# Kernel optimization log

Hardware: AMD Instinct MI355X
Metric: run time of the kernel (lower is better)

## Reference

```python
import jax, jax.numpy as jnp
import numpy as np
import math

N, S, T, D = 4, 2048, 2048, 1024

def setup_inputs() -> dict:
    key = jax.random.key(0)
    ks = jax.random.split(key, 6)
    scale = 1.0 / math.sqrt(D)
    return {
        "query": jax.random.normal(ks[0], (N, S, D), dtype=jnp.float32),
        "key": jax.random.normal(ks[1], (N, T, D), dtype=jnp.float32),
        "value": jax.random.normal(ks[2], (N, T, D), dtype=jnp.float32),
        # causal mask: 1 = attend, 0 = masked out (masked_fill where mask == 0)
        "attn_mask": jnp.tril(jnp.ones((S, T), dtype=jnp.int32)),
        "Wq": jax.random.normal(ks[3], (D, D), dtype=jnp.float32) * scale,
        "Wk": jax.random.normal(ks[4], (D, D), dtype=jnp.float32) * scale,
        "Wv": jax.random.normal(ks[5], (D, D), dtype=jnp.float32) * scale,
    }

def reference(query, key, value, attn_mask, Wq, Wk, Wv):
    # nn.Linear(bias=False): y = x @ W.T
    q = jnp.einsum('nsd,ed->nse', query, Wq)
    k = jnp.einsum('ntd,ed->nte', key, Wk)
    v = jnp.einsum('ntd,ed->nte', value, Wv)
    # scaled dot-product scores [N, S, T]
    dot = jnp.einsum('nse,nte->nst', q, k) / jnp.sqrt(jnp.asarray(D, q.dtype))
    dot = jnp.where(attn_mask == 0, -jnp.inf, dot)
    scores = jax.nn.softmax(dot, axis=-1)
    # dropout is identity in eval mode
    y = jnp.einsum('nst,nte->nse', scores, v)
    return y
```

## Files before the change

### kernel.cpp

```cpp
#include <hip/hip_runtime.h>
#include <math.h>

using u16 = unsigned short;
typedef __attribute__((ext_vector_type(8))) __bf16 bf16x8;
typedef __attribute__((ext_vector_type(4))) float f32x4;
typedef __attribute__((ext_vector_type(4))) float f4v;
typedef __attribute__((ext_vector_type(8))) u16 u16x8;

__device__ __forceinline__ u16 f2bf(float f) {
  unsigned u = __float_as_uint(f);
  u += 0x7fffu + ((u >> 16) & 1u);
  return (u16)(u >> 16);
}

__device__ __forceinline__ void gload16(const void* g, void* l) {
  __builtin_amdgcn_global_load_lds(
      (const __attribute__((address_space(1))) unsigned int*)g,
      (__attribute__((address_space(3))) unsigned int*)l, 16, 0, 0);
}

__device__ __forceinline__ f32x4 MF(bf16x8 a, bf16x8 b, f32x4 c) {
  return __builtin_amdgcn_mfma_f32_16x16x32_bf16(a, b, c, 0, 0, 0);
}

#define BARX() __builtin_amdgcn_s_barrier()
#define LGKM0() asm volatile("s_waitcnt lgkmcnt(0)" ::: "memory")
#define VMW4() asm volatile("s_waitcnt vmcnt(4)" ::: "memory")
#define VMW0() asm volatile("s_waitcnt vmcnt(0)" ::: "memory")

__global__ __launch_bounds__(256) void prep(
    const float* __restrict__ q, const float* __restrict__ v,
    const float* __restrict__ k, const float* __restrict__ Wk,
    const float* __restrict__ Wq, const float* __restrict__ Wv,
    u16* __restrict__ qb, u16* __restrict__ wkT, u16* __restrict__ wqT,
    u16* __restrict__ wv_bf, float* __restrict__ lbuf) {
  __shared__ float t[64][65];
  int b = blockIdx.x;
  if (b < 6144) {
    int z = b >> 11;
    int bb = b & 2047;
    const float* in = (z == 0) ? q : (z == 1) ? v : k;
    size_t i = ((size_t)bb * 256 + threadIdx.x) * 16;
    f4v a0 = *reinterpret_cast<const f4v*>(in + i);
    f4v a1 = *reinterpret_cast<const f4v*>(in + i + 4);
    f4v a2 = *reinterpret_cast<const f4v*>(in + i + 8);
    f4v a3 = *reinterpret_cast<const f4v*>(in + i + 12);
    u16x8 r0, r1;
    r0[0] = f2bf(a0[0]); r0[1] = f2bf(a0[1]); r0[2] = f2bf(a0[2]); r0[3] = f2bf(a0[3]);
    r0[4] = f2bf(a1[0]); r0[5] = f2bf(a1[1]); r0[6] = f2bf(a1[2]); r0[7] = f2bf(a1[3]);
    r1[0] = f2bf(a2[0]); r1[1] = f2bf(a2[1]); r1[2] = f2bf(a2[2]); r1[3] = f2bf(a2[3]);
    r1[4] = f2bf(a3[0]); r1[5] = f2bf(a3[1]); r1[6] = f2bf(a3[2]); r1[7] = f2bf(a3[3]);
    u16* o = qb + (size_t)z * 8388608 + i;
    *reinterpret_cast<u16x8*>(o) = r0;
    *reinterpret_cast<u16x8*>(o + 8) = r1;
  } else if (b < 6656) {
    int c = b - 6144;
    int z = c >> 8, idx = c & 255;
    const float* I = z ? Wq : Wk;
    u16* O = z ? wqT : wkT;
    int c0 = (idx & 15) * 64, r0 = (idx >> 4) * 64;
    int tx = threadIdx.x & 63, ty = threadIdx.x >> 6;
    #pragma unroll
    for (int i = 0; i < 64; i += 4)
      t[ty + i][tx] = I[(size_t)(r0 + ty + i) * 1024 + c0 + tx];
    __syncthreads();
    #pragma unroll
    for (int i = 0; i < 64; i += 4)
      O[(size_t)(c0 + ty + i) * 1024 + r0 + tx] = f2bf(t[tx][ty + i]);
  } else if (b < 6912) {
    int bb = b - 6656;
    size_t i = (size_t)bb * 4096 + threadIdx.x * 16;
    #pragma unroll
    for (int h = 0; h < 2; ++h) {
      f4v a = *reinterpret_cast<const f4v*>(Wv + i + h * 8);
      f4v c = *reinterpret_cast<const f4v*>(Wv + i + h * 8 + 4);
      u16x8 r;
      r[0] = f2bf(a[0]); r[1] = f2bf(a[1]); r[2] = f2bf(a[2]); r[3] = f2bf(a[3]);
      r[4] = f2bf(c[0]); r[5] = f2bf(c[1]); r[6] = f2bf(c[2]); r[7] = f2bf(c[3]);
      *reinterpret_cast<u16x8*>(wv_bf + i + h * 8) = r;
    }
  } else {
    f4v z4 = {0.f, 0.f, 0.f, 0.f};
    #pragma unroll
    for (int j = 0; j < 8; ++j)
      *reinterpret_cast<f4v*>(&lbuf[threadIdx.x * 32 + j * 4]) = z4;
  }
}

__global__ __launch_bounds__(512, 1) void proj256(
    const u16* __restrict__ Xq, const u16* __restrict__ Xv,
    const u16* __restrict__ Mt, const u16* __restrict__ Wv,
    u16* __restrict__ Yq, u16* __restrict__ Vt) {
  int h = blockIdx.x;
  int l = (h & 7) * 32 + (h >> 3);
  const bool wV = l >= 128;
  int li = l & 127;
  int bm, bn;
  const u16 *Ag, *Bg;
  if (!wV) {
    bm = li >> 2; bn = li & 3;
    Ag = Xq + (size_t)bm * 256 * 1024;
    Bg = Mt + (size_t)bn * 256 * 1024;
  } else {
    bm = li & 3; bn = li >> 2;
    Ag = Wv + (size_t)bm * 256 * 1024;
    Bg = Xv + (size_t)bn * 256 * 1024;
  }

  __shared__ __align__(16) char sm[131072];

  const int tid = threadIdx.x;
  const int lane = tid & 63, wv = tid >> 6;
  const int wr = wv >> 2, wc = wv & 3;
  const int fr = lane & 15, hi = lane >> 4, fr7 = lane & 7;
  const int l3 = lane >> 3;
  const int colsw = ((lane & 7) ^ l3) * 8;
  const int lnx16 = lane * 16;

  const u16 *pA[2][2], *pB[2][2];
  int ldsA[2][2], ldsB[2][2];
  #pragma unroll
  for (int hh = 0; hh < 2; ++hh)
    #pragma unroll
    for (int j = 0; j < 2; ++j) {
      int row = hh * 128 + wv * 8 + j * 64 + l3;
      pA[hh][j] = Ag + (size_t)row * 1024 + colsw;
      pB[hh][j] = Bg + (size_t)row * 1024 + colsw;
      ldsA[hh][j] = hh * 16384 + (wv + j * 8) * 1024 + lnx16;
      ldsB[hh][j] = 32768 + ldsA[hh][j];
    }

  const int aBase = wr * 16384 + fr * 128;
  const int bBase = 32768 + (wc >> 1) * 16384 + ((wc & 1) * 64 + fr) * 128;
  const int sl0 = (hi ^ fr7) << 4;
  const int sl1 = ((4 + hi) ^ fr7) << 4;

#define RDA(buf, m, kk) (*(const bf16x8*)((buf) + aBase + (m) * 2048 + ((kk) ? sl1 : sl0)))
#define RDB(buf, n, kk) (*(const bf16x8*)((buf) + bBase + (n) * 2048 + ((kk) ? sl1 : sl0)))

  f32x4 acc[8][4] = {};
  const int nt = 16;

  {
    char* b0 = sm;
    gload16(pA[0][0], b0 + ldsA[0][0]); gload16(pA[0][1], b0 + ldsA[0][1]);
    gload16(pA[1][0], b0 + ldsA[1][0]); gload16(pA[1][1], b0 + ldsA[1][1]);
    gload16(pB[0][0], b0 + ldsB[0][0]); gload16(pB[0][1], b0 + ldsB[0][1]);
    gload16(pB[1][0], b0 + ldsB[1][0]); gload16(pB[1][1], b0 + ldsB[1][1]);
    char* b1 = sm + 65536;
    gload16(pB[0][0] + 64, b1 + ldsB[0][0]); gload16(pB[0][1] + 64, b1 + ldsB[0][1]);
    gload16(pB[1][0] + 64, b1 + ldsB[1][0]); gload16(pB[1][1] + 64, b1 + ldsB[1][1]);
  }
  VMW4();
  BARX();

  for (int t = 0; t < nt; ++t) {
    const int cur = t & 1;
    const char* buf = sm + cur * 65536;
    char* nbuf = sm + (cur ^ 1) * 65536;
    char* cbuf = sm + cur * 65536;
    const bool st1 = (t + 1 < nt), st2 = (t + 2 < nt);
    bf16x8 bf0[4], bf1[4];
    bf16x8 a00, a01, a10, a11;

    a00 = RDA(buf, 0, 0); a01 = RDA(buf, 0, 1);
    a10 = RDA(buf, 1, 0); a11 = RDA(buf, 1, 1);
    #pragma unroll
    for (int n = 0; n < 4; ++n) { bf0[n] = RDB(buf, n, 0); bf1[n] = RDB(buf, n, 1); }
    if (st1) {
      gload16(pA[0][0] + (t + 1) * 64, nbuf + ldsA[0][0]);
      gload16(pA[0][1] + (t + 1) * 64, nbuf + ldsA[0][1]);
    }
    BARX(); LGKM0();
    __builtin_amdgcn_s_setprio(1);
    #pragma unroll
    for (int n = 0; n < 4; ++n) {
      acc[0][n] = MF(a00, bf0[n], acc[0][n]);
      acc[0][n] = MF(a01, bf1[n], acc[0][n]);
      acc[1][n] = MF(a10, bf0[n], acc[1][n]);
      acc[1][n] = MF(a11, bf1[n], acc[1][n]);
    }
    __builtin_amdgcn_s_setprio(0);
    BARX();

    a00 = RDA(buf, 2, 0); a01 = RDA(buf, 2, 1);
    a10 = RDA(buf, 3, 0); a11 = RDA(buf, 3, 1);
    if (st1) {
      gload16(pA[1][0] + (t + 1) * 64, nbuf + ldsA[1][0]);
      gload16(pA[1][1] + (t + 1) * 64, nbuf + ldsA[1][1]);
    }
    if (st2) {
      gload16(pB[0][0] + (t + 2) * 64, cbuf + ldsB[0][0]);
      gload16(pB[0][1] + (t + 2) * 64, cbuf + ldsB[0][1]);
    }
    BARX(); LGKM0();
    __builtin_amdgcn_s_setprio(1);
    #pragma unroll
    for (int n = 0; n < 4; ++n) {
      acc[2][n] = MF(a00, bf0[n], acc[2][n]);
      acc[2][n] = MF(a01, bf1[n], acc[2][n]);
      acc[3][n] = MF(a10, bf0[n], acc[3][n]);
      acc[3][n] = MF(a11, bf1[n], acc[3][n]);
    }
    __builtin_amdgcn_s_setprio(0);
    BARX();

    a00 = RDA(buf, 4, 0); a01 = RDA(buf, 4, 1);
    a10 = RDA(buf, 5, 0); a11 = RDA(buf, 5, 1);
    if (st2) {
      gload16(pB[1][0] + (t + 2) * 64, cbuf + ldsB[1][0]);
      gload16(pB[1][1] + (t + 2) * 64, cbuf + ldsB[1][1]);
    }
    BARX(); LGKM0();
    __builtin_amdgcn_s_setprio(1);
    #pragma unroll
    for (int n = 0; n < 4; ++n) {
      acc[4][n] = MF(a00, bf0[n], acc[4][n]);
      acc[4][n] = MF(a01, bf1[n], acc[4][n]);
      acc[5][n] = MF(a10, bf0[n], acc[5][n]);
      acc[5][n] = MF(a11, bf1[n], acc[5][n]);
    }
    __builtin_amdgcn_s_setprio(0);
    BARX();

    a00 = RDA(buf, 6, 0); a01 = RDA(buf, 6, 1);
    a10 = RDA(buf, 7, 0); a11 = RDA(buf, 7, 1);
    if (st2) { VMW4(); } else if (st1) { VMW0(); }
    BARX(); LGKM0();
    __builtin_amdgcn_s_setprio(1);
    #pragma unroll
    for (int n = 0; n < 4; ++n) {
      acc[6][n] = MF(a00, bf0[n], acc[6][n]);
      acc[6][n] = MF(a01, bf1[n], acc[6][n]);
      acc[7][n] = MF(a10, bf0[n], acc[7][n]);
      acc[7][n] = MF(a11, bf1[n], acc[7][n]);
    }
    __builtin_amdgcn_s_setprio(0);
    BARX();
  }

  if (!wV) {
    const int row0 = bm * 256 + wr * 128 + hi * 4;
    const int col0 = bn * 256 + wc * 64 + fr;
    #pragma unroll
    for (int m = 0; m < 8; ++m)
      #pragma unroll
      for (int n = 0; n < 4; ++n)
        #pragma unroll
        for (int j = 0; j < 4; ++j)
          Yq[(size_t)(row0 + m * 16 + j) * 1024 + (col0 + n * 16)] =
              f2bf(acc[m][n][j]);
  } else {
    const int e0 = bm * 256 + wr * 128 + hi * 4;
    const int t0 = (bn & 7) * 256 + wc * 64 + fr;
    const size_t zoff = (size_t)(bn >> 3) * (1024 * 2048);
    #pragma unroll
    for (int m = 0; m < 8; ++m)
      #pragma unroll
      for (int n = 0; n < 4; ++n)
        #pragma unroll
        for (int j = 0; j < 4; ++j)
          Vt[zoff + (size_t)(e0 + m * 16 + j) * 2048 + (t0 + n * 16)] =
              f2bf(acc[m][n][j]);
  }
#undef RDA
#undef RDB
}

template<typename OutT, int MODE>
__global__ __launch_bounds__(512) void gemm_bt8(
    const u16* __restrict__ A, const u16* __restrict__ B, OutT* __restrict__ C,
    int K, int lda, int ldb, int ldc,
    size_t sA, size_t sB, size_t sC, float alpha, float* __restrict__ lbuf) {
  int bn, bm, bz = 0;
  int kEnd = K;
  if (MODE == 0) {
    bm = blockIdx.x >> 3;
    bn = blockIdx.x & 7;
  } else if (MODE == 1) {
    int h = blockIdx.x;
    int l = (h & 7) * 68 + (h >> 3);
    bz = l / 136;
    int t = l % 136;
    bm = (int)((sqrtf(8.f * (float)t + 1.f) - 1.f) * 0.5f);
    while ((bm + 1) * (bm + 2) / 2 <= t) ++bm;
    while (bm * (bm + 1) / 2 > t) --bm;
    bn = t - bm * (bm + 1) / 2;
  } else {
    int l = blockIdx.x;
    bm = 15 - (l >> 5);
    int rest = l & 31;
    bz = rest >> 3;
    bn = rest & 7;
    kEnd = (K < (bm + 1) * 128) ? K : (bm + 1) * 128;
  }
  const u16* Ag = A + sA * bz + (size_t)bm * 128 * lda;
  const u16* Bg = B + sB * bz + (size_t)bn * 128 * ldb;
  OutT* Cg = C + sC * bz;

  __shared__ __align__(16) u16 As[2][128 * 32];
  __shared__ __align__(16) u16 Bs[2][128 * 32];

  const int tid = threadIdx.x;
  const int lane = tid & 63, wv = tid >> 6;
  const int wr = wv >> 2, wc = wv & 3;
  const int fr = lane & 15, kq = (lane >> 4) * 8;
  const int g4 = (lane >> 4) * 4;

  const int e0 = wv * 512 + lane * 8;
  const int r0 = e0 >> 5, c0 = e0 & 31;
  const u16* a0 = Ag + (size_t)r0 * lda + c0;
  const u16* b0 = Bg + (size_t)r0 * ldb + c0;

  f32x4 acc[4][2] = {};
  const int nt = kEnd / 32;

  gload16(a0, &As[0][wv * 512]);
  gload16(b0, &Bs[0][wv * 512]);
  __syncthreads();

  for (int t = 0; t < nt; ++t) {
    const int cur = t & 1;
    if (t + 1 < nt) {
      const int k0 = (t + 1) * 32;
      gload16(a0 + k0, &As[cur ^ 1][wv * 512]);
      gload16(b0 + k0, &Bs[cur ^ 1][wv * 512]);
    }
    bf16x8 af[4], bfv[2];
    #pragma unroll
    for (int m = 0; m < 4; ++m)
      af[m] = *reinterpret_cast<const bf16x8*>(&As[cur][(wr * 64 + m * 16 + fr) * 32 + kq]);
    #pragma unroll
    for (int n = 0; n < 2; ++n)
      bfv[n] = *reinterpret_cast<const bf16x8*>(&Bs[cur][(wc * 32 + n * 16 + fr) * 32 + kq]);
    #pragma unroll
    for (int m = 0; m < 4; ++m)
      #pragma unroll
      for (int n = 0; n < 2; ++n)
        acc[m][n] = MF(af[m], bfv[n], acc[m][n]);
    __syncthreads();
  }

  if constexpr (MODE == 1) {
    float psum[4][4];
    #pragma unroll
    for (int m = 0; m < 4; ++m)
      #pragma unroll
      for (int j = 0; j < 4; ++j) {
        int tr = wr * 64 + g4 + m * 16 + j;
        float rs = 0.f;
        #pragma unroll
        for (int n = 0; n < 2; ++n) {
          int tc = wc * 32 + fr + n * 16;
          float p = 0.f;
          if (!(bm == bn && tc > tr)) p = __expf(acc[m][n][j] * alpha);
          Cg[(size_t)(bm * 128 + tr) * ldc + (bn * 128 + tc)] = f2bf(p);
          rs += p;
        }
        psum[m][j] = rs;
      }
    #pragma unroll
    for (int o = 1; o < 16; o <<= 1)
      #pragma unroll
      for (int m = 0; m < 4; ++m)
        #pragma unroll
        for (int j = 0; j < 4; ++j)
          psum[m][j] += __shfl_xor(psum[m][j], o, 64);
    float* lsum = (float*)As;
    if (fr == 0)
      #pragma unroll
      for (int m = 0; m < 4; ++m)
        #pragma unroll
        for (int j = 0; j < 4; ++j)
          lsum[wc * 128 + wr * 64 + g4 + m * 16 + j] = psum[m][j];
    __syncthreads();
    if (tid < 128) {
      float s = lsum[tid] + lsum[128 + tid] + lsum[256 + tid] + lsum[384 + tid];
      atomicAdd(&lbuf[(size_t)bz * 2048 + bm * 128 + tid], s);
    }
    return;
  }

  float il[4][4];
  if constexpr (MODE == 2) {
    #pragma unroll
    for (int m = 0; m < 4; ++m)
      #pragma unroll
      for (int j = 0; j < 4; ++j)
        il[m][j] = 1.0f / lbuf[(size_t)bz * 2048 + bm * 128 + wr * 64 + g4 + m * 16 + j];
  }

  const int row0 = bm * 128 + wr * 64 + g4;
  const int col0 = bn * 128 + wc * 32 + fr;
  #pragma unroll
  for (int m = 0; m < 4; ++m)
    #pragma unroll
    for (int n = 0; n < 2; ++n) {
      #pragma unroll
      for (int j = 0; j < 4; ++j) {
        float val;
        if constexpr (MODE == 2) val = acc[m][n][j] * il[m][j];
        else val = acc[m][n][j] * alpha;
        size_t idx = (size_t)(row0 + m * 16 + j) * ldc + (col0 + n * 16);
        if constexpr (sizeof(OutT) == 2) Cg[idx] = f2bf(val);
        else Cg[idx] = val;
      }
    }
}

extern "C" void kernel_launch(void* const* d_in, const int* in_sizes, int n_in,
                              void* d_out, int out_size, void* d_ws, size_t ws_size,
                              hipStream_t stream) {
  const float* q  = (const float*)d_in[0];
  const float* k  = (const float*)d_in[1];
  const float* v  = (const float*)d_in[2];
  const float* Wq = (const float*)d_in[4];
  const float* Wk = (const float*)d_in[5];
  const float* Wv = (const float*)d_in[6];
  float* out = (float*)d_out;
  char* ws = (char*)d_ws;

  const size_t MB = 1024ull * 1024ull;
  u16* sc   = (u16*)ws;
  u16* qb   = (u16*)ws;
  u16* xk   = (u16*)(ws + 32 * MB);
  u16* wsl  = (u16*)(ws + 48 * MB);
  u16* wkT  = (u16*)(ws + 52 * MB);
  u16* wqT  = (u16*)(ws + 54 * MB);
  u16* Vt   = (u16*)(ws + 56 * MB);
  u16* Yq   = (u16*)(ws + 72 * MB);
  float* lb = (float*)(ws + 88 * MB);
  (void)in_sizes; (void)n_in; (void)out_size; (void)ws_size;

  prep<<<6913, 256, 0, stream>>>(q, v, k, Wk, Wq, Wv, qb, wkT, wqT,
                                 wsl + 1048576, lb);

  gemm_bt8<u16, 0><<<64, 512, 0, stream>>>(
      wkT, wqT, wsl, 1024, 1024, 1024, 1024, 0, 0, 0, 1.0f, nullptr);

  proj256<<<256, 512, 0, stream>>>(qb, qb + 8388608, wsl, wsl + 1048576,
                                   Yq, Vt);

  gemm_bt8<u16, 1><<<544, 512, 0, stream>>>(
      Yq, xk, sc, 1024, 1024, 1024, 2048,
      (size_t)2048 * 1024, (size_t)2048 * 1024, (size_t)2048 * 2048, 0.03125f,
      lb);

  gemm_bt8<float, 2><<<512, 512, 0, stream>>>(
      sc, Vt, out, 2048, 2048, 2048, 1024,
      (size_t)2048 * 2048, (size_t)1024 * 2048, (size_t)2048 * 1024, 1.0f,
      lb);
}
```

Baseline: 156.6 us.

## Use 256x256 tiled GEMMs for scores and PV with split-K atomics

```diff
diff --git a/kernel.cpp b/kernel.cpp
--- a/kernel.cpp
+++ b/kernel.cpp
@@ -33,7 +33,7 @@
     const float* __restrict__ k, const float* __restrict__ Wk,
     const float* __restrict__ Wq, const float* __restrict__ Wv,
     u16* __restrict__ qb, u16* __restrict__ wkT, u16* __restrict__ wqT,
-    u16* __restrict__ wv_bf, float* __restrict__ lbuf) {
+    u16* __restrict__ wv_bf, float* __restrict__ lbuf, float* __restrict__ O) {
   __shared__ float t[64][65];
   int b = blockIdx.x;
   if (b < 6144) {
@@ -57,7 +57,7 @@
     int c = b - 6144;
     int z = c >> 8, idx = c & 255;
     const float* I = z ? Wq : Wk;
-    u16* O = z ? wqT : wkT;
+    u16* O2 = z ? wqT : wkT;
     int c0 = (idx & 15) * 64, r0 = (idx >> 4) * 64;
     int tx = threadIdx.x & 63, ty = threadIdx.x >> 6;
     #pragma unroll
@@ -66,7 +66,7 @@
     __syncthreads();
     #pragma unroll
     for (int i = 0; i < 64; i += 4)
-      O[(size_t)(c0 + ty + i) * 1024 + r0 + tx] = f2bf(t[tx][ty + i]);
+      O2[(size_t)(c0 + ty + i) * 1024 + r0 + tx] = f2bf(t[tx][ty + i]);
   } else if (b < 6912) {
     int bb = b - 6656;
     size_t i = (size_t)bb * 4096 + threadIdx.x * 16;
@@ -79,11 +79,20 @@
       r[4] = f2bf(c[0]); r[5] = f2bf(c[1]); r[6] = f2bf(c[2]); r[7] = f2bf(c[3]);
       *reinterpret_cast<u16x8*>(wv_bf + i + h * 8) = r;
     }
-  } else {
+  } else if (b == 6912) {
     f4v z4 = {0.f, 0.f, 0.f, 0.f};
     #pragma unroll
     for (int j = 0; j < 8; ++j)
       *reinterpret_cast<f4v*>(&lbuf[threadIdx.x * 32 + j * 4]) = z4;
+  } else {
+    int c = b - 6913;
+    int bz = c >> 8, bb = c & 255;
+    float* p = O + (size_t)bz * 2097152 + 1048576 +
+               (size_t)bb * 4096 + threadIdx.x * 16;
+    f4v z4 = {0.f, 0.f, 0.f, 0.f};
+    #pragma unroll
+    for (int j = 0; j < 4; ++j)
+      *reinterpret_cast<f4v*>(p + j * 4) = z4;
   }
 }
 
@@ -267,36 +276,244 @@
 #undef RDB
 }
 
-template<typename OutT, int MODE>
-__global__ __launch_bounds__(512) void gemm_bt8(
-    const u16* __restrict__ A, const u16* __restrict__ B, OutT* __restrict__ C,
-    int K, int lda, int ldb, int ldc,
-    size_t sA, size_t sB, size_t sC, float alpha, float* __restrict__ lbuf) {
-  int bn, bm, bz = 0;
-  int kEnd = K;
-  if (MODE == 0) {
-    bm = blockIdx.x >> 3;
-    bn = blockIdx.x & 7;
-  } else if (MODE == 1) {
-    int h = blockIdx.x;
-    int l = (h & 7) * 68 + (h >> 3);
-    bz = l / 136;
-    int t = l % 136;
-    bm = (int)((sqrtf(8.f * (float)t + 1.f) - 1.f) * 0.5f);
-    while ((bm + 1) * (bm + 2) / 2 <= t) ++bm;
-    while (bm * (bm + 1) / 2 > t) --bm;
-    bn = t - bm * (bm + 1) / 2;
+template<int MODE>
+__global__ __launch_bounds__(512, 1) void g256(
+    const u16* __restrict__ A, const u16* __restrict__ B,
+    u16* __restrict__ P, float* __restrict__ O, float* __restrict__ lbuf) {
+  int h = blockIdx.x;
+  int bm, bn, bz, nt, lda, ldb;
+  bool split = false;
+  const u16 *Ag, *Bg;
+  if (MODE == 1) {
+    int l = (h & 7) * 18 + (h >> 3);
+    bz = l / 36;
+    int tt = l % 36;
+    bm = (int)((sqrtf(8.f * tt + 1.f) - 1.f) * 0.5f);
+    while ((bm + 1) * (bm + 2) / 2 <= tt) ++bm;
+    while (bm * (bm + 1) / 2 > tt) --bm;
+    bn = tt - bm * (bm + 1) / 2;
+    lda = 1024; ldb = 1024; nt = 16;
+    Ag = A + (size_t)bz * 2097152 + (size_t)bm * 256 * 1024;
+    Bg = B + (size_t)bz * 2097152 + (size_t)bn * 256 * 1024;
   } else {
-    int l = blockIdx.x;
-    bm = 15 - (l >> 5);
-    int rest = l & 31;
-    bz = rest >> 3;
-    bn = rest & 7;
-    kEnd = (K < (bm + 1) * 128) ? K : (bm + 1) * 128;
-  }
-  const u16* Ag = A + sA * bz + (size_t)bm * 128 * lda;
-  const u16* Bg = B + sB * bz + (size_t)bn * 128 * ldb;
-  OutT* Cg = C + sC * bz;
+    int l = (h & 7) * 24 + (h >> 3);
+    bz = l / 48;
+    int r = l % 48;
+    bn = r & 3;
+    int idx = r >> 2, sk = 0;
+    if (idx < 4) bm = idx;
+    else { int e = idx - 4; bm = 4 + (e >> 1); sk = e & 1; }
+    split = (bm >= 4);
+    int klen = split ? (bm + 1) * 128 : (bm + 1) * 256;
+    int kbase = sk * klen;
+    nt = klen >> 6;
+    lda = 2048; ldb = 2048;
+    Ag = A + (size_t)bz * 4194304 + (size_t)bm * 256 * 2048 + kbase;
+    Bg = B + (size_t)bz * 2097152 + (size_t)bn * 256 * 2048 + kbase;
+  }
+
+  __shared__ __align__(16) char sm[131072];
+
+  const int tid = threadIdx.x;
+  const int lane = tid & 63, wv = tid >> 6;
+  const int wr = wv >> 2, wc = wv & 3;
+  const int fr = lane & 15, hi = lane >> 4, fr7 = lane & 7;
+  const int l3 = lane >> 3;
+  const int colsw = ((lane & 7) ^ l3) * 8;
+  const int lnx16 = lane * 16;
+
+  const u16 *pA[2][2], *pB[2][2];
+  int ldsA[2][2], ldsB[2][2];
+  #pragma unroll
+  for (int hh = 0; hh < 2; ++hh)
+    #pragma unroll
+    for (int j = 0; j < 2; ++j) {
+      int row = hh * 128 + wv * 8 + j * 64 + l3;
+      pA[hh][j] = Ag + (size_t)row * lda + colsw;
+      pB[hh][j] = Bg + (size_t)row * ldb + colsw;
+      ldsA[hh][j] = hh * 16384 + (wv + j * 8) * 1024 + lnx16;
+      ldsB[hh][j] = 32768 + ldsA[hh][j];
+    }
+
+  const int aBase = wr * 16384 + fr * 128;
+  const int bBase = 32768 + (wc >> 1) * 16384 + ((wc & 1) * 64 + fr) * 128;
+  const int sl0 = (hi ^ fr7) << 4;
+  const int sl1 = ((4 + hi) ^ fr7) << 4;
+
+#define RDA(buf, m, kk) (*(const bf16x8*)((buf) + aBase + (m) * 2048 + ((kk) ? sl1 : sl0)))
+#define RDB(buf, n, kk) (*(const bf16x8*)((buf) + bBase + (n) * 2048 + ((kk) ? sl1 : sl0)))
+
+  f32x4 acc[8][4] = {};
+
+  {
+    char* b0 = sm;
+    gload16(pA[0][0], b0 + ldsA[0][0]); gload16(pA[0][1], b0 + ldsA[0][1]);
+    gload16(pA[1][0], b0 + ldsA[1][0]); gload16(pA[1][1], b0 + ldsA[1][1]);
+    gload16(pB[0][0], b0 + ldsB[0][0]); gload16(pB[0][1], b0 + ldsB[0][1]);
+    gload16(pB[1][0], b0 + ldsB[1][0]); gload16(pB[1][1], b0 + ldsB[1][1]);
+    char* b1 = sm + 65536;
+    gload16(pB[0][0] + 64, b1 + ldsB[0][0]); gload16(pB[0][1] + 64, b1 + ldsB[0][1]);
+    gload16(pB[1][0] + 64, b1 + ldsB[1][0]); gload16(pB[1][1] + 64, b1 + ldsB[1][1]);
+  }
+  VMW4();
+  BARX();
+
+  for (int t = 0; t < nt; ++t) {
+    const int cur = t & 1;
+    const char* buf = sm + cur * 65536;
+    char* nbuf = sm + (cur ^ 1) * 65536;
+    char* cbuf = sm + cur * 65536;
+    const bool st1 = (t + 1 < nt), st2 = (t + 2 < nt);
+    bf16x8 bf0[4], bf1[4];
+    bf16x8 a00, a01, a10, a11;
+
+    a00 = RDA(buf, 0, 0); a01 = RDA(buf, 0, 1);
+    a10 = RDA(buf, 1, 0); a11 = RDA(buf, 1, 1);
+    #pragma unroll
+    for (int n = 0; n < 4; ++n) { bf0[n] = RDB(buf, n, 0); bf1[n] = RDB(buf, n, 1); }
+    if (st1) {
+      gload16(pA[0][0] + (t + 1) * 64, nbuf + ldsA[0][0]);
+      gload16(pA[0][1] + (t + 1) * 64, nbuf + ldsA[0][1]);
+    }
+    BARX(); LGKM0();
+    __builtin_amdgcn_s_setprio(1);
+    #pragma unroll
+    for (int n = 0; n < 4; ++n) {
+      acc[0][n] = MF(a00, bf0[n], acc[0][n]);
+      acc[0][n] = MF(a01, bf1[n], acc[0][n]);
+      acc[1][n] = MF(a10, bf0[n], acc[1][n]);
+      acc[1][n] = MF(a11, bf1[n], acc[1][n]);
+    }
+    __builtin_amdgcn_s_setprio(0);
+    BARX();
+
+    a00 = RDA(buf, 2, 0); a01 = RDA(buf, 2, 1);
+    a10 = RDA(buf, 3, 0); a11 = RDA(buf, 3, 1);
+    if (st1) {
+      gload16(pA[1][0] + (t + 1) * 64, nbuf + ldsA[1][0]);
+      gload16(pA[1][1] + (t + 1) * 64, nbuf + ldsA[1][1]);
+    }
+    if (st2) {
+      gload16(pB[0][0] + (t + 2) * 64, cbuf + ldsB[0][0]);
+      gload16(pB[0][1] + (t + 2) * 64, cbuf + ldsB[0][1]);
+    }
+    BARX(); LGKM0();
+    __builtin_amdgcn_s_setprio(1);
+    #pragma unroll
+    for (int n = 0; n < 4; ++n) {
+      acc[2][n] = MF(a00, bf0[n], acc[2][n]);
+      acc[2][n] = MF(a01, bf1[n], acc[2][n]);
+      acc[3][n] = MF(a10, bf0[n], acc[3][n]);
+      acc[3][n] = MF(a11, bf1[n], acc[3][n]);
+    }
+    __builtin_amdgcn_s_setprio(0);
+    BARX();
+
+    a00 = RDA(buf, 4, 0); a01 = RDA(buf, 4, 1);
+    a10 = RDA(buf, 5, 0); a11 = RDA(buf, 5, 1);
+    if (st2) {
+      gload16(pB[1][0] + (t + 2) * 64, cbuf + ldsB[1][0]);
+      gload16(pB[1][1] + (t + 2) * 64, cbuf + ldsB[1][1]);
+    }
+    BARX(); LGKM0();
+    __builtin_amdgcn_s_setprio(1);
+    #pragma unroll
+    for (int n = 0; n < 4; ++n) {
+      acc[4][n] = MF(a00, bf0[n], acc[4][n]);
+      acc[4][n] = MF(a01, bf1[n], acc[4][n]);
+      acc[5][n] = MF(a10, bf0[n], acc[5][n]);
+      acc[5][n] = MF(a11, bf1[n], acc[5][n]);
+    }
+    __builtin_amdgcn_s_setprio(0);
+    BARX();
+
+    a00 = RDA(buf, 6, 0); a01 = RDA(buf, 6, 1);
+    a10 = RDA(buf, 7, 0); a11 = RDA(buf, 7, 1);
+    if (st2) { VMW4(); } else if (st1) { VMW0(); }
+    BARX(); LGKM0();
+    __builtin_amdgcn_s_setprio(1);
+    #pragma unroll
+    for (int n = 0; n < 4; ++n) {
+      acc[6][n] = MF(a00, bf0[n], acc[6][n]);
+      acc[6][n] = MF(a01, bf1[n], acc[6][n]);
+      acc[7][n] = MF(a10, bf0[n], acc[7][n]);
+      acc[7][n] = MF(a11, bf1[n], acc[7][n]);
+    }
+    __builtin_amdgcn_s_setprio(0);
+    BARX();
+  }
+#undef RDA
+#undef RDB
+
+  if constexpr (MODE == 1) {
+    u16* Pg = P + (size_t)bz * 4194304;
+    const int tr0 = bm * 256 + wr * 128 + hi * 4;
+    const int tc0 = bn * 256 + wc * 64 + fr;
+    float rsum[8][4];
+    #pragma unroll
+    for (int m = 0; m < 8; ++m)
+      #pragma unroll
+      for (int j = 0; j < 4; ++j) {
+        int tr = tr0 + m * 16 + j;
+        float rs = 0.f;
+        #pragma unroll
+        for (int n = 0; n < 4; ++n) {
+          int tc = tc0 + n * 16;
+          float p = 0.f;
+          if (!(bm == bn && tc > tr)) p = __expf(acc[m][n][j] * 0.03125f);
+          Pg[(size_t)tr * 2048 + tc] = f2bf(p);
+          rs += p;
+        }
+        rsum[m][j] = rs;
+      }
+    #pragma unroll
+    for (int o = 1; o < 16; o <<= 1)
+      #pragma unroll
+      for (int m = 0; m < 8; ++m)
+        #pragma unroll
+        for (int j = 0; j < 4; ++j)
+          rsum[m][j] += __shfl_xor(rsum[m][j], o, 64);
+    float* lsum = (float*)sm;
+    if (fr == 0)
+      #pragma unroll
+      for (int m = 0; m < 8; ++m)
+        #pragma unroll
+        for (int j = 0; j < 4; ++j)
+          lsum[wc * 256 + wr * 128 + hi * 4 + m * 16 + j] = rsum[m][j];
+    __syncthreads();
+    if (tid < 256) {
+      float s = lsum[tid] + lsum[256 + tid] + lsum[512 + tid] + lsum[768 + tid];
+      atomicAdd(&lbuf[(size_t)bz * 2048 + bm * 256 + tid], s);
+    }
+  } else {
+    float* Og = O + (size_t)bz * 2097152;
+    const int row0 = bm * 256 + wr * 128 + hi * 4;
+    const int col0 = bn * 256 + wc * 64 + fr;
+    float il[8][4];
+    #pragma unroll
+    for (int m = 0; m < 8; ++m)
+      #pragma unroll
+      for (int j = 0; j < 4; ++j)
+        il[m][j] = 1.0f / lbuf[(size_t)bz * 2048 + row0 + m * 16 + j];
+    #pragma unroll
+    for (int m = 0; m < 8; ++m)
+      #pragma unroll
+      for (int n = 0; n < 4; ++n)
+        #pragma unroll
+        for (int j = 0; j < 4; ++j) {
+          float vv = acc[m][n][j] * il[m][j];
+          size_t idx = (size_t)(row0 + m * 16 + j) * 1024 + (col0 + n * 16);
+          if (split) unsafeAtomicAdd(&Og[idx], vv);
+          else Og[idx] = vv;
+        }
+  }
+}
+
+__global__ __launch_bounds__(512) void gemm_mt(
+    const u16* __restrict__ A, const u16* __restrict__ B, u16* __restrict__ C) {
+  int bm = blockIdx.x >> 3, bn = blockIdx.x & 7;
+  const u16* Ag = A + (size_t)bm * 128 * 1024;
+  const u16* Bg = B + (size_t)bn * 128 * 1024;
 
   __shared__ __align__(16) u16 As[2][128 * 32];
   __shared__ __align__(16) u16 Bs[2][128 * 32];
@@ -309,19 +526,18 @@
 
   const int e0 = wv * 512 + lane * 8;
   const int r0 = e0 >> 5, c0 = e0 & 31;
-  const u16* a0 = Ag + (size_t)r0 * lda + c0;
-  const u16* b0 = Bg + (size_t)r0 * ldb + c0;
+  const u16* a0 = Ag + (size_t)r0 * 1024 + c0;
+  const u16* b0 = Bg + (size_t)r0 * 1024 + c0;
 
   f32x4 acc[4][2] = {};
-  const int nt = kEnd / 32;
 
   gload16(a0, &As[0][wv * 512]);
   gload16(b0, &Bs[0][wv * 512]);
   __syncthreads();
 
-  for (int t = 0; t < nt; ++t) {
+  for (int t = 0; t < 32; ++t) {
     const int cur = t & 1;
-    if (t + 1 < nt) {
+    if (t + 1 < 32) {
       const int k0 = (t + 1) * 32;
       gload16(a0 + k0, &As[cur ^ 1][wv * 512]);
       gload16(b0 + k0, &Bs[cur ^ 1][wv * 512]);
@@ -339,55 +555,6 @@
       for (int n = 0; n < 2; ++n)
         acc[m][n] = MF(af[m], bfv[n], acc[m][n]);
     __syncthreads();
-  }
-
-  if constexpr (MODE == 1) {
-    float psum[4][4];
-    #pragma unroll
-    for (int m = 0; m < 4; ++m)
-      #pragma unroll
-      for (int j = 0; j < 4; ++j) {
-        int tr = wr * 64 + g4 + m * 16 + j;
-        float rs = 0.f;
-        #pragma unroll
-        for (int n = 0; n < 2; ++n) {
-          int tc = wc * 32 + fr + n * 16;
-          float p = 0.f;
-          if (!(bm == bn && tc > tr)) p = __expf(acc[m][n][j] * alpha);
-          Cg[(size_t)(bm * 128 + tr) * ldc + (bn * 128 + tc)] = f2bf(p);
-          rs += p;
-        }
-        psum[m][j] = rs;
-      }
-    #pragma unroll
-    for (int o = 1; o < 16; o <<= 1)
-      #pragma unroll
-      for (int m = 0; m < 4; ++m)
-        #pragma unroll
-        for (int j = 0; j < 4; ++j)
-          psum[m][j] += __shfl_xor(psum[m][j], o, 64);
-    float* lsum = (float*)As;
-    if (fr == 0)
-      #pragma unroll
-      for (int m = 0; m < 4; ++m)
-        #pragma unroll
-        for (int j = 0; j < 4; ++j)
-          lsum[wc * 128 + wr * 64 + g4 + m * 16 + j] = psum[m][j];
-    __syncthreads();
-    if (tid < 128) {
-      float s = lsum[tid] + lsum[128 + tid] + lsum[256 + tid] + lsum[384 + tid];
-      atomicAdd(&lbuf[(size_t)bz * 2048 + bm * 128 + tid], s);
-    }
-    return;
-  }
-
-  float il[4][4];
-  if constexpr (MODE == 2) {
-    #pragma unroll
-    for (int m = 0; m < 4; ++m)
-      #pragma unroll
-      for (int j = 0; j < 4; ++j)
-        il[m][j] = 1.0f / lbuf[(size_t)bz * 2048 + bm * 128 + wr * 64 + g4 + m * 16 + j];
   }
 
   const int row0 = bm * 128 + wr * 64 + g4;
@@ -395,17 +562,11 @@
   #pragma unroll
   for (int m = 0; m < 4; ++m)
     #pragma unroll
-    for (int n = 0; n < 2; ++n) {
-      #pragma unroll
-      for (int j = 0; j < 4; ++j) {
-        float val;
-        if constexpr (MODE == 2) val = acc[m][n][j] * il[m][j];
-        else val = acc[m][n][j] * alpha;
-        size_t idx = (size_t)(row0 + m * 16 + j) * ldc + (col0 + n * 16);
-        if constexpr (sizeof(OutT) == 2) Cg[idx] = f2bf(val);
-        else Cg[idx] = val;
-      }
-    }
+    for (int n = 0; n < 2; ++n)
+      #pragma unroll
+      for (int j = 0; j < 4; ++j)
+        C[(size_t)(row0 + m * 16 + j) * 1024 + (col0 + n * 16)] =
+            f2bf(acc[m][n][j]);
 }
 
 extern "C" void kernel_launch(void* const* d_in, const int* in_sizes, int n_in,
@@ -432,22 +593,15 @@
   float* lb = (float*)(ws + 88 * MB);
   (void)in_sizes; (void)n_in; (void)out_size; (void)ws_size;
 
-  prep<<<6913, 256, 0, stream>>>(q, v, k, Wk, Wq, Wv, qb, wkT, wqT,
-                                 wsl + 1048576, lb);
-
-  gemm_bt8<u16, 0><<<64, 512, 0, stream>>>(
-      wkT, wqT, wsl, 1024, 1024, 1024, 1024, 0, 0, 0, 1.0f, nullptr);
+  prep<<<7937, 256, 0, stream>>>(q, v, k, Wk, Wq, Wv, qb, wkT, wqT,
+                                 wsl + 1048576, lb, out);
+
+  gemm_mt<<<64, 512, 0, stream>>>(wkT, wqT, wsl);
 
   proj256<<<256, 512, 0, stream>>>(qb, qb + 8388608, wsl, wsl + 1048576,
                                    Yq, Vt);
 
-  gemm_bt8<u16, 1><<<544, 512, 0, stream>>>(
-      Yq, xk, sc, 1024, 1024, 1024, 2048,
-      (size_t)2048 * 1024, (size_t)2048 * 1024, (size_t)2048 * 2048, 0.03125f,
-      lb);
-
-  gemm_bt8<float, 2><<<512, 512, 0, stream>>>(
-      sc, Vt, out, 2048, 2048, 2048, 1024,
-      (size_t)2048 * 2048, (size_t)1024 * 2048, (size_t)2048 * 1024, 1.0f,
-      lb);
-}
+  g256<1><<<144, 512, 0, stream>>>(Yq, xk, sc, nullptr, lb);
+
+  g256<2><<<192, 512, 0, stream>>>(sc, Vt, nullptr, out, lb);
+}
```

After: 168.7 us. 1.08x slower.

## Triple-buffer GEMM LDS loads with one barrier per k-step; merge prep conversion blocks

Applied to the files above, without the earlier changes.

```diff
diff --git a/kernel.cpp b/kernel.cpp
--- a/kernel.cpp
+++ b/kernel.cpp
@@ -24,8 +24,10 @@
 }
 
 #define BARX() __builtin_amdgcn_s_barrier()
+#define SCHED0() __builtin_amdgcn_sched_barrier(0)
 #define LGKM0() asm volatile("s_waitcnt lgkmcnt(0)" ::: "memory")
 #define VMW4() asm volatile("s_waitcnt vmcnt(4)" ::: "memory")
+#define VMW2() asm volatile("s_waitcnt vmcnt(2)" ::: "memory")
 #define VMW0() asm volatile("s_waitcnt vmcnt(0)" ::: "memory")
 
 __global__ __launch_bounds__(256) void prep(
@@ -36,25 +38,26 @@
     u16* __restrict__ wv_bf, float* __restrict__ lbuf) {
   __shared__ float t[64][65];
   int b = blockIdx.x;
-  if (b < 6144) {
-    int z = b >> 11;
-    int bb = b & 2047;
-    const float* in = (z == 0) ? q : (z == 1) ? v : k;
-    size_t i = ((size_t)bb * 256 + threadIdx.x) * 16;
-    f4v a0 = *reinterpret_cast<const f4v*>(in + i);
-    f4v a1 = *reinterpret_cast<const f4v*>(in + i + 4);
-    f4v a2 = *reinterpret_cast<const f4v*>(in + i + 8);
-    f4v a3 = *reinterpret_cast<const f4v*>(in + i + 12);
-    u16x8 r0, r1;
-    r0[0] = f2bf(a0[0]); r0[1] = f2bf(a0[1]); r0[2] = f2bf(a0[2]); r0[3] = f2bf(a0[3]);
-    r0[4] = f2bf(a1[0]); r0[5] = f2bf(a1[1]); r0[6] = f2bf(a1[2]); r0[7] = f2bf(a1[3]);
-    r1[0] = f2bf(a2[0]); r1[1] = f2bf(a2[1]); r1[2] = f2bf(a2[2]); r1[3] = f2bf(a2[3]);
-    r1[4] = f2bf(a3[0]); r1[5] = f2bf(a3[1]); r1[6] = f2bf(a3[2]); r1[7] = f2bf(a3[3]);
-    u16* o = qb + (size_t)z * 8388608 + i;
-    *reinterpret_cast<u16x8*>(o) = r0;
-    *reinterpret_cast<u16x8*>(o + 8) = r1;
-  } else if (b < 6656) {
-    int c = b - 6144;
+  if (b < 2048) {
+    size_t off = ((size_t)b * 256 + threadIdx.x) * 16;
+    #pragma unroll
+    for (int z = 0; z < 3; ++z) {
+      const float* in = (z == 0) ? q : (z == 1) ? v : k;
+      f4v a0 = *reinterpret_cast<const f4v*>(in + off);
+      f4v a1 = *reinterpret_cast<const f4v*>(in + off + 4);
+      f4v a2 = *reinterpret_cast<const f4v*>(in + off + 8);
+      f4v a3 = *reinterpret_cast<const f4v*>(in + off + 12);
+      u16x8 r0, r1;
+      r0[0] = f2bf(a0[0]); r0[1] = f2bf(a0[1]); r0[2] = f2bf(a0[2]); r0[3] = f2bf(a0[3]);
+      r0[4] = f2bf(a1[0]); r0[5] = f2bf(a1[1]); r0[6] = f2bf(a1[2]); r0[7] = f2bf(a1[3]);
+      r1[0] = f2bf(a2[0]); r1[1] = f2bf(a2[1]); r1[2] = f2bf(a2[2]); r1[3] = f2bf(a2[3]);
+      r1[4] = f2bf(a3[0]); r1[5] = f2bf(a3[1]); r1[6] = f2bf(a3[2]); r1[7] = f2bf(a3[3]);
+      u16* o = qb + (size_t)z * 8388608 + off;
+      *reinterpret_cast<u16x8*>(o) = r0;
+      *reinterpret_cast<u16x8*>(o + 8) = r1;
+    }
+  } else if (b < 2560) {
+    int c = b - 2048;
     int z = c >> 8, idx = c & 255;
     const float* I = z ? Wq : Wk;
     u16* O = z ? wqT : wkT;
@@ -67,8 +70,8 @@
     #pragma unroll
     for (int i = 0; i < 64; i += 4)
       O[(size_t)(c0 + ty + i) * 1024 + r0 + tx] = f2bf(t[tx][ty + i]);
-  } else if (b < 6912) {
-    int bb = b - 6656;
+  } else if (b < 2816) {
+    int bb = b - 2560;
     size_t i = (size_t)bb * 4096 + threadIdx.x * 16;
     #pragma unroll
     for (int h = 0; h < 2; ++h) {
@@ -298,8 +301,8 @@
   const u16* Bg = B + sB * bz + (size_t)bn * 128 * ldb;
   OutT* Cg = C + sC * bz;
 
-  __shared__ __align__(16) u16 As[2][128 * 32];
-  __shared__ __align__(16) u16 Bs[2][128 * 32];
+  __shared__ __align__(16) u16 As[3][4096];
+  __shared__ __align__(16) u16 Bs[3][4096];
 
   const int tid = threadIdx.x;
   const int lane = tid & 63, wv = tid >> 6;
@@ -317,15 +320,30 @@
 
   gload16(a0, &As[0][wv * 512]);
   gload16(b0, &Bs[0][wv * 512]);
-  __syncthreads();
-
+  if (nt > 1) {
+    gload16(a0 + 32, &As[1][wv * 512]);
+    gload16(b0 + 32, &Bs[1][wv * 512]);
+    VMW2();
+  } else {
+    VMW0();
+  }
+  BARX();
+  SCHED0();
+
+  int cur = 0;
   for (int t = 0; t < nt; ++t) {
-    const int cur = t & 1;
-    if (t + 1 < nt) {
-      const int k0 = (t + 1) * 32;
-      gload16(a0 + k0, &As[cur ^ 1][wv * 512]);
-      gload16(b0 + k0, &Bs[cur ^ 1][wv * 512]);
-    }
+    if (t + 2 < nt) {
+      const int nxt = (cur + 2 > 2) ? cur - 1 : cur + 2;
+      const int k0 = (t + 2) * 32;
+      gload16(a0 + k0, &As[nxt][wv * 512]);
+      gload16(b0 + k0, &Bs[nxt][wv * 512]);
+      VMW4();
+    } else if (t + 1 < nt) {
+      VMW2();
+    } else {
+      VMW0();
+    }
+    SCHED0();
     bf16x8 af[4], bfv[2];
     #pragma unroll
     for (int m = 0; m < 4; ++m)
@@ -333,12 +351,16 @@
     #pragma unroll
     for (int n = 0; n < 2; ++n)
       bfv[n] = *reinterpret_cast<const bf16x8*>(&Bs[cur][(wc * 32 + n * 16 + fr) * 32 + kq]);
+    LGKM0();
+    SCHED0();
+    BARX();
+    SCHED0();
     #pragma unroll
     for (int m = 0; m < 4; ++m)
       #pragma unroll
       for (int n = 0; n < 2; ++n)
         acc[m][n] = MF(af[m], bfv[n], acc[m][n]);
-    __syncthreads();
+    cur = (cur == 2) ? 0 : cur + 1;
   }
 
   if constexpr (MODE == 1) {
@@ -367,6 +389,7 @@
         for (int j = 0; j < 4; ++j)
           psum[m][j] += __shfl_xor(psum[m][j], o, 64);
     float* lsum = (float*)As;
+    __syncthreads();
     if (fr == 0)
       #pragma unroll
       for (int m = 0; m < 4; ++m)
@@ -432,7 +455,7 @@
   float* lb = (float*)(ws + 88 * MB);
   (void)in_sizes; (void)n_in; (void)out_size; (void)ws_size;
 
-  prep<<<6913, 256, 0, stream>>>(q, v, k, Wk, Wq, Wv, qb, wkT, wqT,
+  prep<<<2817, 256, 0, stream>>>(q, v, k, Wk, Wq, Wv, qb, wkT, wqT,
                                  wsl + 1048576, lb);
 
   gemm_bt8<u16, 0><<<64, 512, 0, stream>>>(
```

Result: slower. 162.1 us (+3.5%).

## Split-K the causal PV GEMM into two halves with atomic accumulation

Applied to the files above, without the earlier changes.

```diff
diff --git a/kernel.cpp b/kernel.cpp
--- a/kernel.cpp
+++ b/kernel.cpp
@@ -33,7 +33,7 @@
     const float* __restrict__ k, const float* __restrict__ Wk,
     const float* __restrict__ Wq, const float* __restrict__ Wv,
     u16* __restrict__ qb, u16* __restrict__ wkT, u16* __restrict__ wqT,
-    u16* __restrict__ wv_bf, float* __restrict__ lbuf) {
+    u16* __restrict__ wv_bf, float* __restrict__ lbuf, float* __restrict__ O) {
   __shared__ float t[64][65];
   int b = blockIdx.x;
   if (b < 6144) {
@@ -57,7 +57,7 @@
     int c = b - 6144;
     int z = c >> 8, idx = c & 255;
     const float* I = z ? Wq : Wk;
-    u16* O = z ? wqT : wkT;
+    u16* O2 = z ? wqT : wkT;
     int c0 = (idx & 15) * 64, r0 = (idx >> 4) * 64;
     int tx = threadIdx.x & 63, ty = threadIdx.x >> 6;
     #pragma unroll
@@ -66,7 +66,7 @@
     __syncthreads();
     #pragma unroll
     for (int i = 0; i < 64; i += 4)
-      O[(size_t)(c0 + ty + i) * 1024 + r0 + tx] = f2bf(t[tx][ty + i]);
+      O2[(size_t)(c0 + ty + i) * 1024 + r0 + tx] = f2bf(t[tx][ty + i]);
   } else if (b < 6912) {
     int bb = b - 6656;
     size_t i = (size_t)bb * 4096 + threadIdx.x * 16;
@@ -79,11 +79,18 @@
       r[4] = f2bf(c[0]); r[5] = f2bf(c[1]); r[6] = f2bf(c[2]); r[7] = f2bf(c[3]);
       *reinterpret_cast<u16x8*>(wv_bf + i + h * 8) = r;
     }
-  } else {
+  } else if (b == 6912) {
     f4v z4 = {0.f, 0.f, 0.f, 0.f};
     #pragma unroll
     for (int j = 0; j < 8; ++j)
       *reinterpret_cast<f4v*>(&lbuf[threadIdx.x * 32 + j * 4]) = z4;
+  } else {
+    int c = b - 6913;
+    float* p = O + (size_t)c * 4096 + threadIdx.x * 16;
+    f4v z4 = {0.f, 0.f, 0.f, 0.f};
+    #pragma unroll
+    for (int j = 0; j < 4; ++j)
+      *reinterpret_cast<f4v*>(p + j * 4) = z4;
   }
 }
 
@@ -273,7 +280,7 @@
     int K, int lda, int ldb, int ldc,
     size_t sA, size_t sB, size_t sC, float alpha, float* __restrict__ lbuf) {
   int bn, bm, bz = 0;
-  int kEnd = K;
+  int kEnd = K, kBase = 0;
   if (MODE == 0) {
     bm = blockIdx.x >> 3;
     bn = blockIdx.x & 7;
@@ -288,14 +295,17 @@
     bn = t - bm * (bm + 1) / 2;
   } else {
     int l = blockIdx.x;
-    bm = 15 - (l >> 5);
-    int rest = l & 31;
-    bz = rest >> 3;
+    bm = 15 - (l >> 6);
+    int rest = l & 63;
+    int sk = rest >> 5;
+    bz = (rest >> 3) & 3;
     bn = rest & 7;
-    kEnd = (K < (bm + 1) * 128) ? K : (bm + 1) * 128;
-  }
-  const u16* Ag = A + sA * bz + (size_t)bm * 128 * lda;
-  const u16* Bg = B + sB * bz + (size_t)bn * 128 * ldb;
+    int half = (bm + 1) * 64;
+    kBase = sk * half;
+    kEnd = half;
+  }
+  const u16* Ag = A + sA * bz + (size_t)bm * 128 * lda + kBase;
+  const u16* Bg = B + sB * bz + (size_t)bn * 128 * ldb + kBase;
   OutT* Cg = C + sC * bz;
 
   __shared__ __align__(16) u16 As[2][128 * 32];
@@ -398,12 +408,14 @@
     for (int n = 0; n < 2; ++n) {
       #pragma unroll
       for (int j = 0; j < 4; ++j) {
-        float val;
-        if constexpr (MODE == 2) val = acc[m][n][j] * il[m][j];
-        else val = acc[m][n][j] * alpha;
         size_t idx = (size_t)(row0 + m * 16 + j) * ldc + (col0 + n * 16);
-        if constexpr (sizeof(OutT) == 2) Cg[idx] = f2bf(val);
-        else Cg[idx] = val;
+        if constexpr (MODE == 2) {
+          unsafeAtomicAdd((float*)&Cg[idx], acc[m][n][j] * il[m][j]);
+        } else {
+          float val = acc[m][n][j] * alpha;
+          if constexpr (sizeof(OutT) == 2) Cg[idx] = f2bf(val);
+          else Cg[idx] = val;
+        }
       }
     }
 }
@@ -432,8 +444,8 @@
   float* lb = (float*)(ws + 88 * MB);
   (void)in_sizes; (void)n_in; (void)out_size; (void)ws_size;
 
-  prep<<<6913, 256, 0, stream>>>(q, v, k, Wk, Wq, Wv, qb, wkT, wqT,
-                                 wsl + 1048576, lb);
+  prep<<<8961, 256, 0, stream>>>(q, v, k, Wk, Wq, Wv, qb, wkT, wqT,
+                                 wsl + 1048576, lb, out);
 
   gemm_bt8<u16, 0><<<64, 512, 0, stream>>>(
       wkT, wqT, wsl, 1024, 1024, 1024, 1024, 0, 0, 0, 1.0f, nullptr);
@@ -446,7 +458,7 @@
       (size_t)2048 * 1024, (size_t)2048 * 1024, (size_t)2048 * 2048, 0.03125f,
       lb);
 
-  gemm_bt8<float, 2><<<512, 512, 0, stream>>>(
+  gemm_bt8<float, 2><<<1024, 512, 0, stream>>>(
       sc, Vt, out, 2048, 2048, 2048, 1024,
       (size_t)2048 * 2048, (size_t)1024 * 2048, (size_t)2048 * 1024, 1.0f,
       lb);
```

Result: slower. 193.6 us (+23.7%).
